# Kernel tuning notes

Hardware: AMD Instinct MI355X
Metric: run time of the kernel (lower is better)

The kernel has to match this reference:

```python
import jax, jax.numpy as jnp
import numpy as np

B, L, HID = 2, 2048, 512
NUM_HEADS = 8
HEAD_DIM = HID // NUM_HEADS
GAP_ROWS = 33   # num_time_gap_buckets + 1
DUR_ROWS = 17   # num_duration_buckets + 1
NEG = -1e9      # finite stand-in for -inf (grad-safe, masked probs ~0)


def setup_inputs() -> dict:
    key = jax.random.key(0)
    ks = jax.random.split(key, 16)
    s = 1.0 / np.sqrt(HID)
    x = jax.random.normal(ks[0], (B, L, HID), dtype=jnp.float32)
    attention_mask = jax.random.randint(ks[1], (B, L), 0, 2, dtype=jnp.int32)
    time_gap_bucket_ids = jax.random.randint(ks[2], (B, L), 0, GAP_ROWS, dtype=jnp.int32)
    duration_bucket_ids = jax.random.randint(ks[3], (B, L), 0, DUR_ROWS, dtype=jnp.int32)
    Wq = jax.random.normal(ks[4], (HID, HID), dtype=jnp.float32) * s
    bq = jnp.zeros((HID,), jnp.float32)
    Wk = jax.random.normal(ks[5], (HID, HID), dtype=jnp.float32) * s
    bk = jnp.zeros((HID,), jnp.float32)
    Wv = jax.random.normal(ks[6], (HID, HID), dtype=jnp.float32) * s
    bv = jnp.zeros((HID,), jnp.float32)
    Wo = jax.random.normal(ks[7], (HID, HID), dtype=jnp.float32) * s
    bo = jnp.zeros((HID,), jnp.float32)
    # bias tables: padding_idx=0 row kept at zero, rest random for a meaningful test
    gap_emb = jax.random.normal(ks[8], (GAP_ROWS, NUM_HEADS), dtype=jnp.float32) * 0.1
    gap_emb = gap_emb.at[0].set(0.0)
    dur_emb = jax.random.normal(ks[9], (DUR_ROWS, NUM_HEADS), dtype=jnp.float32) * 0.1
    dur_emb = dur_emb.at[0].set(0.0)
    return dict(x=x, attention_mask=attention_mask,
                time_gap_bucket_ids=time_gap_bucket_ids,
                duration_bucket_ids=duration_bucket_ids,
                Wq=Wq, bq=bq, Wk=Wk, bk=bk, Wv=Wv, bv=bv, Wo=Wo, bo=bo,
                gap_emb=gap_emb, dur_emb=dur_emb)


def reference(x, attention_mask, time_gap_bucket_ids, duration_bucket_ids,
              Wq, bq, Wk, bk, Wv, bv, Wo, bo, gap_emb, dur_emb):
    b, l, hid = x.shape
    h, d = NUM_HEADS, HEAD_DIM
    def split_heads(t):  # (B,L,HID) -> (B,h,L,d)
        return t.reshape(b, l, h, d).transpose(0, 2, 1, 3)
    Q = split_heads(x @ Wq + bq)
    K = split_heads(x @ Wk + bk)
    V = split_heads(x @ Wv + bv)
    scores = jnp.einsum('bhqd,bhkd->bhqk', Q, K) / jnp.sqrt(jnp.float32(d))
    # relative time-gap bias: (B,L,L) bucket lookup -> (B,h,L,L)
    rel = jnp.abs(time_gap_bucket_ids[:, :, None] - time_gap_bucket_ids[:, None, :])
    rel = jnp.clip(rel, 0, GAP_ROWS - 1)
    gap_bias = gap_emb[rel]                       # (B,L,L,h)
    scores = scores + gap_bias.transpose(0, 3, 1, 2)
    # per-key duration bias: (B,L,h) -> (B,h,1,L)
    dur_bias = dur_emb[duration_bucket_ids]       # (B,L,h)
    scores = scores + dur_bias.transpose(0, 2, 1)[:, :, None, :]
    pad = (attention_mask == 0)[:, None, None, :]  # (B,1,1,L) over keys
    scores = jnp.where(pad, NEG, scores)
    attn = jax.nn.softmax(scores, axis=-1)
    out = jnp.einsum('bhqk,bhkd->bhqd', attn, V)
    out = out.transpose(0, 2, 1, 3).reshape(b, l, hid)
    return out @ Wo + bo
```

## Files before the change

### kernel.cpp

```cpp
#include <hip/hip_runtime.h>
#include <cmath>

typedef unsigned short u16;
typedef unsigned int   u32;
typedef __attribute__((ext_vector_type(2))) unsigned uintx2;
typedef __attribute__((ext_vector_type(4))) float    floatx4;
typedef __attribute__((ext_vector_type(4))) unsigned uintx4;
typedef __attribute__((ext_vector_type(8))) __bf16   bf16x8;

#define MFMA16(a, b, c) __builtin_amdgcn_mfma_f32_16x16x32_bf16((a), (b), (c), 0, 0, 0)

__device__ __forceinline__ u16 f2bf(float f) {
    union { float f; u32 u; } v; v.f = f;
    u32 u = v.u;
    return (u16)((u + 0x7FFFu + ((u >> 16) & 1u)) >> 16);
}

__device__ __forceinline__ bf16x8 ld_frag(const u16* p) {
    uintx4 t = *(const uintx4*)p;
    return __builtin_bit_cast(bf16x8, t);
}

#if __has_builtin(__builtin_amdgcn_exp2f)
#define EXP2F(x) __builtin_amdgcn_exp2f(x)
#else
#define EXP2F(x) exp2f(x)
#endif

typedef __attribute__((address_space(3))) unsigned       lds_u32;
typedef __attribute__((address_space(1))) const unsigned glb_u32;
__device__ __forceinline__ void gl_lds16(const void* g, void* l) {
    __builtin_amdgcn_global_load_lds((glb_u32*)(uintptr_t)g, (lds_u32*)(uintptr_t)l, 16, 0, 0);
}

#define LOG2E   1.4426950408889634f
#define QSCALE  0.18033688011112043f

__global__ __launch_bounds__(256) void prep_kernel(
        const float* __restrict__ x, const int* __restrict__ gap_ids,
        const int* __restrict__ dur_ids, const int* __restrict__ amask,
        const float* __restrict__ gap_emb, const float* __restrict__ dur_emb,
        const float* __restrict__ Wq, const float* __restrict__ Wk,
        const float* __restrict__ Wv, const float* __restrict__ Wo,
        u16* __restrict__ Xb, u16* __restrict__ Qe, u16* __restrict__ Ke,
        u16* __restrict__ WqT, u16* __restrict__ WkT,
        u16* __restrict__ WvT, u16* __restrict__ WoT) {
    __shared__ u16 T[64][72];
    int bid = blockIdx.x, tid = threadIdx.x;
    if (bid < 1024) {
        int idx = bid * 256 + tid;
        const float* src = x + (size_t)idx * 8;
        uintx4 o;
        o.x = f2bf(src[0]) | ((u32)f2bf(src[1]) << 16);
        o.y = f2bf(src[2]) | ((u32)f2bf(src[3]) << 16);
        o.z = f2bf(src[4]) | ((u32)f2bf(src[5]) << 16);
        o.w = f2bf(src[6]) | ((u32)f2bf(src[7]) << 16);
        *(uintx4*)(Xb + (size_t)idx * 8) = o;
    } else if (bid < 2048) {
        int ri = (bid - 1024) * 32 + (tid >> 3);
        int l = ri & 2047;
        int b = ri >> 14;
        int ch = tid & 7;
        int gq = gap_ids[b * 2048 + l];
        u16 lg = f2bf(LOG2E);
        u16 vals[8];
        for (int e = 0; e < 8; e++) {
            int j = ch * 8 + e;
            vals[e] = (j == gq || j == 33) ? lg : (u16)0;
        }
        *(uintx4*)(Qe + (size_t)ri * 128 + (8 + ch) * 8) = *(uintx4*)vals;
    } else if (bid < 3072) {
        int ri = (bid - 2048) * 32 + (tid >> 3);
        int bh = ri >> 11, l = ri & 2047;
        int b = bh >> 3, h = bh & 7;
        int ch = tid & 7;
        int gk = gap_ids[b * 2048 + l];
        int did = dur_ids[b * 2048 + l];
        int msk = amask[b * 2048 + l];
        float kval = msk ? dur_emb[did * 8 + h] : -1e9f;
        u16 vals[8];
        for (int e = 0; e < 8; e++) {
            int j = ch * 8 + e;
            float v;
            if (j <= 32) { int d = j - gk; d = d < 0 ? -d : d; v = gap_emb[d * 8 + h]; }
            else if (j == 33) v = kval;
            else v = 0.f;
            vals[e] = f2bf(v);
        }
        int phys = 8 | (ch ^ (l & 7));
        *(uintx4*)(Ke + (size_t)ri * 128 + phys * 8) = *(uintx4*)vals;
    } else {
        int bid2 = bid - 3072;
        int mat = bid2 >> 6, t8 = bid2 & 63;
        int n0 = (t8 & 7) * 64, k0 = (t8 >> 3) * 64;
        const float* W = (mat == 0) ? Wq : (mat == 1) ? Wk : (mat == 2) ? Wv : Wo;
        u16* WT = (mat == 0) ? WqT : (mat == 1) ? WkT : (mat == 2) ? WvT : WoT;
        int r = tid >> 4, cq = tid & 15;
        for (int rr = 0; rr < 4; rr++) {
            int row = r + rr * 16;
            floatx4 s = *(const floatx4*)&W[(size_t)(k0 + row) * 512 + n0 + cq * 4];
            T[cq * 4 + 0][row] = f2bf(s.x);
            T[cq * 4 + 1][row] = f2bf(s.y);
            T[cq * 4 + 2][row] = f2bf(s.z);
            T[cq * 4 + 3][row] = f2bf(s.w);
        }
        __syncthreads();
        for (int p = 0; p < 2; p++) {
            int idx = p * 256 + tid;
            int c = idx >> 3, ch = idx & 7;
            *(uintx4*)&WT[(size_t)(n0 + c) * 512 + k0 + ch * 8] = *(const uintx4*)&T[c][ch * 8];
        }
    }
}

__global__ __launch_bounds__(256) void gemm_qkv(
        const u16* __restrict__ Xb,
        const u16* __restrict__ WqT, const u16* __restrict__ WkT, const u16* __restrict__ WvT,
        const float* __restrict__ bq, const float* __restrict__ bk, const float* __restrict__ bv,
        u16* __restrict__ Qe, u16* __restrict__ Ke, u16* __restrict__ Vt) {
    __shared__ u16 smem[12288];
    u16* As = smem;
    u16* Bs = smem + 8192;

    int tid = threadIdx.x;
    int m0 = blockIdx.x * 128;
    int gy = blockIdx.y;
    int mat = gy >> 3, hh = gy & 7;
    int ncol0 = hh * 64;
    const u16* Bt = (mat == 0) ? WqT : (mat == 1) ? WkT : WvT;
    const float* bias = (mat == 0) ? bq : (mat == 1) ? bk : bv;

    int lane = tid & 63, w = tid >> 6, lo = lane & 15, hi = lane >> 4;
    int wm = w >> 1, wn = w & 1;
    floatx4 acc[4][2] = {};

    for (int kb = 0; kb < 8; kb++) {
        int k0 = kb * 64;
        __syncthreads();
        for (int it = 0; it < 4; it++) {
            int c = it * 256 + tid;
            int row = c >> 3, ch = c & 7;
            gl_lds16((const char*)Xb + ((size_t)(m0 + row) * 512 + k0) * 2 + ch * 16,
                     (char*)As + c * 16);
        }
        for (int it = 0; it < 2; it++) {
            int c = it * 256 + tid;
            int row = c >> 3, ch = c & 7;
            gl_lds16((const char*)Bt + ((size_t)(ncol0 + row) * 512 + k0) * 2 + ch * 16,
                     (char*)Bs + c * 16);
        }
        __syncthreads();
        for (int s = 0; s < 2; s++) {
            bf16x8 a[4], b[2];
            for (int i = 0; i < 4; i++)
                a[i] = ld_frag(&As[(64 * wm + 16 * i + lo) * 64 + s * 32 + hi * 8]);
            for (int j = 0; j < 2; j++)
                b[j] = ld_frag(&Bs[(32 * wn + 16 * j + lo) * 64 + s * 32 + hi * 8]);
            for (int i = 0; i < 4; i++)
                for (int j = 0; j < 2; j++)
                    acc[i][j] = MFMA16(a[i], b[j], acc[i][j]);
        }
    }

    int bb = m0 >> 11, l0 = m0 & 2047;
    __syncthreads();

    if (mat < 2) {
        u16* Ot = smem;
        for (int j = 0; j < 2; j++) {
            int col = 32 * wn + 16 * j + lo;
            float bval = bias[ncol0 + col];
            for (int i = 0; i < 4; i++) {
                int row = 64 * wm + 16 * i + 4 * hi;
                for (int r = 0; r < 4; r++) {
                    float v = acc[i][j][r] + bval;
                    if (mat == 0) v *= QSCALE;
                    Ot[(row + r) * 72 + col] = f2bf(v);
                }
            }
        }
        __syncthreads();
        for (int p = 0; p < 4; p++) {
            int cc = p * 256 + tid;
            int row = cc >> 3, ch = cc & 7;
            int lrow = l0 + row;
            size_t rowi = (size_t)(bb * 8 + hh) * 2048 + lrow;
            int ch2 = (mat == 1) ? (ch ^ (lrow & 7)) : ch;
            u16* dstp = (mat == 0) ? Qe : Ke;
            *(uintx4*)(dstp + rowi * 128 + ch2 * 8) = *(const uintx4*)(Ot + row * 72 + ch * 8);
        }
    } else {
        u16* Ot = smem;
        for (int j = 0; j < 2; j++) {
            int dc = 32 * wn + 16 * j + lo;
            float bval = bias[ncol0 + dc];
            for (int i = 0; i < 4; i++) {
                int row = 64 * wm + 16 * i + 4 * hi;
                for (int r = 0; r < 4; r++)
                    Ot[dc * 136 + row + r] = f2bf(acc[i][j][r] + bval);
            }
        }
        __syncthreads();
        for (int p = 0; p < 4; p++) {
            int cc4 = p * 256 + tid;
            int dc = cc4 >> 4, c16 = cc4 & 15;
            int g64 = c16 >> 3, phys = c16 & 7;
            int mlog = phys ^ (dc & 7);
            int g = mlog >> 2, q = mlog & 3;
            int base = g64 * 64 + 32 * g + 4 * q;
            uintx2 lo4 = *(const uintx2*)(Ot + dc * 136 + base);
            uintx2 hi4 = *(const uintx2*)(Ot + dc * 136 + base + 16);
            uintx4 t; t.x = lo4.x; t.y = lo4.y; t.z = hi4.x; t.w = hi4.y;
            size_t dst = ((size_t)(bb * 8 + hh) * 64 + dc) * 2048 + l0 + g64 * 64 + phys * 8;
            *(uintx4*)(Vt + dst) = t;
        }
    }
}

__global__ __launch_bounds__(256, 3) void flash_attn(
        const u16* __restrict__ Qe, const u16* __restrict__ Ke, const u16* __restrict__ Vt,
        float* __restrict__ Opart, float* __restrict__ Lpart) {
    __shared__ u16 Ks[2][64 * 128];
    __shared__ u16 Vs[2][64 * 64];

    int tid = threadIdx.x, lane = tid & 63, w = tid >> 6, lo = lane & 15, hi = lane >> 4;
    int qt2 = blockIdx.x, bh = blockIdx.y, sp = blockIdx.z;
    int sw = lo & 7;

    bf16x8 bq_[2][4];
    for (int g = 0; g < 2; g++) {
        size_t qrow = ((size_t)bh * 2048 + qt2 * 128 + g * 64 + 16 * w + lo) * 128;
        for (int kc = 0; kc < 4; kc++) bq_[g][kc] = ld_frag(&Qe[qrow + kc * 32 + hi * 8]);
    }

    floatx4 O[2][4] = {};
    floatx4 Lacc[2] = {};
    uintx4 onesu; onesu.x = 0x3F803F80u; onesu.y = 0x3F803F80u; onesu.z = 0x3F803F80u; onesu.w = 0x3F803F80u;
    bf16x8 ones = __builtin_bit_cast(bf16x8, onesu);

    const u16* KeB = Ke + (size_t)bh * 2048 * 128;
    const u16* VtB = Vt + (size_t)bh * 64 * 2048;

    int kbeg = sp * 16, kend = kbeg + 16;

#define STAGE(KT, BUF) do {                                                        \
        int k0_ = (KT) * 64;                                                       \
        const char* gk_ = (const char*)(KeB + (size_t)k0_ * 128);                  \
        char* lk_ = (char*)Ks[BUF];                                                \
        for (int r2 = 0; r2 < 4; r2++)                                             \
            gl_lds16(gk_ + r2 * 4096 + tid * 16, lk_ + r2 * 4096 + tid * 16);      \
        for (int p2 = 0; p2 < 2; p2++) {                                           \
            int c_ = p2 * 256 + tid;                                               \
            int row_ = c_ >> 3, ch_ = c_ & 7;                                      \
            gl_lds16((const char*)(VtB + (size_t)row_ * 2048 + k0_) + ch_ * 16,    \
                     (char*)Vs[BUF] + c_ * 16);                                    \
        }                                                                          \
    } while (0)

    int cur = 0;
    STAGE(kbeg, 0);
    for (int kt = kbeg; kt < kend; kt++) {
        __syncthreads();
        if (kt + 1 < kend) STAGE(kt + 1, cur ^ 1);

        const u16* Ksc = Ks[cur];
        const u16* Vsc = Vs[cur];

        floatx4 sf[2][4] = {};
        for (int t = 0; t < 4; t++) {
            const u16* krow = &Ksc[(16 * t + lo) * 128];
            for (int kc = 0; kc < 4; kc++) {
                int cc = kc * 4 + hi;
                int pc = (cc & 8) | ((cc & 7) ^ sw);
                bf16x8 a = ld_frag(&krow[pc * 8]);
                sf[0][t] = MFMA16(a, bq_[0][kc], sf[0][t]);
                sf[1][t] = MFMA16(a, bq_[1][kc], sf[1][t]);
            }
        }

        bf16x8 af[2][2];
        for (int g = 0; g < 2; g++) {
            u32 pk[4][2];
            for (int t = 0; t < 4; t++) {
                float p0 = EXP2F(sf[g][t][0]);
                float p1 = EXP2F(sf[g][t][1]);
                float p2 = EXP2F(sf[g][t][2]);
                float p3 = EXP2F(sf[g][t][3]);
                u32 u0 = __builtin_bit_cast(u32, p0) + 0x8000u;
                u32 u1 = __builtin_bit_cast(u32, p1) + 0x8000u;
                u32 u2 = __builtin_bit_cast(u32, p2) + 0x8000u;
                u32 u3 = __builtin_bit_cast(u32, p3) + 0x8000u;
                pk[t][0] = __builtin_amdgcn_perm(u1, u0, 0x07060302);
                pk[t][1] = __builtin_amdgcn_perm(u3, u2, 0x07060302);
            }
            for (int tp = 0; tp < 2; tp++) {
                uintx4 av;
                av.x = pk[2 * tp][0]; av.y = pk[2 * tp][1];
                av.z = pk[2 * tp + 1][0]; av.w = pk[2 * tp + 1][1];
                af[g][tp] = __builtin_bit_cast(bf16x8, av);
            }
        }

        for (int tp = 0; tp < 2; tp++) {
            Lacc[0] = MFMA16(af[0][tp], ones, Lacc[0]);
            Lacc[1] = MFMA16(af[1][tp], ones, Lacc[1]);
            for (int u = 0; u < 4; u++) {
                const u16* vrow = &Vsc[(16 * u + lo) * 64];
                int m = (4 * tp + hi) ^ sw;
                bf16x8 bv = ld_frag(&vrow[m * 8]);
                O[0][u] = MFMA16(af[0][tp], bv, O[0][u]);
                O[1][u] = MFMA16(af[1][tp], bv, O[1][u]);
            }
        }
        cur ^= 1;
    }
#undef STAGE

    for (int g = 0; g < 2; g++) {
        int qt = 2 * qt2 + g;
        size_t obase = (((size_t)sp * 16 + bh) * 32 + qt) * 4096;
        for (int u = 0; u < 4; u++)
            for (int r = 0; r < 4; r++)
                Opart[obase + (size_t)(16 * w + 4 * hi + r) * 64 + 16 * u + lo] = O[g][u][r];
        if (lo == 0) {
            size_t lbase = (((size_t)sp * 16 + bh) * 32 + qt) * 64;
            for (int r = 0; r < 4; r++) Lpart[lbase + 16 * w + 4 * hi + r] = Lacc[g][r];
        }
    }
}

__global__ __launch_bounds__(256) void combine_kernel(const float* __restrict__ Opart,
                                                      const float* __restrict__ Lpart,
                                                      u16* __restrict__ Ob) {
    int idx = blockIdx.x * 256 + threadIdx.x;
    int d4 = idx & 15;
    int q = (idx >> 4) & 2047;
    int bh = idx >> 15;
    int qt = q >> 6, qr = q & 63;
    size_t b0 = ((size_t)bh * 32 + qt) * 4096 + qr * 64 + d4 * 4;
    floatx4 o0 = *(const floatx4*)&Opart[b0];
    floatx4 o1 = *(const floatx4*)&Opart[b0 + 2097152];
    size_t lb = ((size_t)bh * 32 + qt) * 64 + qr;
    float rl = 1.0f / (Lpart[lb] + Lpart[lb + 32768]);
    uintx2 pk2;
    pk2.x = f2bf((o0.x + o1.x) * rl) | ((u32)f2bf((o0.y + o1.y) * rl) << 16);
    pk2.y = f2bf((o0.z + o1.z) * rl) | ((u32)f2bf((o0.w + o1.w) * rl) << 16);
    int bb = bh >> 3, h = bh & 7;
    *(uintx2*)&Ob[((size_t)(bb * 2048 + q)) * 512 + h * 64 + d4 * 4] = pk2;
}

__global__ __launch_bounds__(256) void gemm_out(
        const u16* __restrict__ Ob, const u16* __restrict__ WoT,
        const float* __restrict__ bo, float* __restrict__ out) {
    __shared__ u16 As[64][72];
    __shared__ u16 Bs[64][72];
    int tid = threadIdx.x;
    int m0 = blockIdx.x * 64;
    int n0 = blockIdx.y * 64;
    int lane = tid & 63, w = tid >> 6, lo = lane & 15, hi = lane >> 4;
    floatx4 acc[4] = {};

    for (int kb = 0; kb < 8; kb++) {
        __syncthreads();
        for (int c = tid; c < 512; c += 256) {
            int row = c >> 3, cc = c & 7;
            *(uintx4*)&As[row][cc * 8] =
                *(const uintx4*)&Ob[(size_t)(m0 + row) * 512 + kb * 64 + cc * 8];
            *(uintx4*)&Bs[row][cc * 8] =
                *(const uintx4*)&WoT[(size_t)(n0 + row) * 512 + kb * 64 + cc * 8];
        }
        __syncthreads();
        for (int s = 0; s < 2; s++) {
            bf16x8 a = ld_frag(&As[16 * w + lo][8 * hi + 32 * s]);
            for (int t = 0; t < 4; t++) {
                bf16x8 b = ld_frag(&Bs[16 * t + lo][8 * hi + 32 * s]);
                acc[t] = MFMA16(a, b, acc[t]);
            }
        }
    }
    for (int t = 0; t < 4; t++) {
        int n = n0 + 16 * t + lo;
        float bval = bo[n];
        for (int r = 0; r < 4; r++) {
            int mrow = m0 + 16 * w + 4 * hi + r;
            out[(size_t)mrow * 512 + n] = acc[t][r] + bval;
        }
    }
}

extern "C" void kernel_launch(void* const* d_in, const int* in_sizes, int n_in,
                              void* d_out, int out_size, void* d_ws, size_t ws_size,
                              hipStream_t stream) {
    const float* x     = (const float*)d_in[0];
    const int*   amask = (const int*)d_in[1];
    const int*   gids  = (const int*)d_in[2];
    const int*   dids  = (const int*)d_in[3];
    const float* Wq    = (const float*)d_in[4];
    const float* bq    = (const float*)d_in[5];
    const float* Wk    = (const float*)d_in[6];
    const float* bk    = (const float*)d_in[7];
    const float* Wv    = (const float*)d_in[8];
    const float* bv    = (const float*)d_in[9];
    const float* Wo    = (const float*)d_in[10];
    const float* bo    = (const float*)d_in[11];
    const float* gap_emb = (const float*)d_in[12];
    const float* dur_emb = (const float*)d_in[13];
    float* out = (float*)d_out;

    char* ws = (char*)d_ws;
    u16*   Qe    = (u16*)(ws + 0);
    u16*   Ke    = (u16*)(ws + 8388608);
    u16*   Vt    = (u16*)(ws + 16777216);
    float* Opart = (float*)(ws + 20971520);
    float* Lpart = (float*)(ws + 37748736);
    u16*   Ob    = (u16*)(ws + 38010880);
    u16*   WoT   = (u16*)(ws + 42205184);
    u16*   Xb    = (u16*)(ws + 20971520);
    u16*   WqT   = (u16*)(ws + 25165824);
    u16*   WkT   = (u16*)(ws + 25690112);
    u16*   WvT   = (u16*)(ws + 26214400);

    hipLaunchKernelGGL(prep_kernel, dim3(3328), dim3(256), 0, stream,
                       x, gids, dids, amask, gap_emb, dur_emb,
                       Wq, Wk, Wv, Wo, Xb, Qe, Ke, WqT, WkT, WvT, WoT);
    hipLaunchKernelGGL(gemm_qkv, dim3(32, 24), dim3(256), 0, stream,
                       Xb, WqT, WkT, WvT, bq, bk, bv, Qe, Ke, Vt);
    hipLaunchKernelGGL(flash_attn, dim3(16, 16, 2), dim3(256), 0, stream,
                       Qe, Ke, Vt, Opart, Lpart);
    hipLaunchKernelGGL(combine_kernel, dim3(2048), dim3(256), 0, stream,
                       Opart, Lpart, Ob);
    hipLaunchKernelGGL(gemm_out, dim3(64, 8), dim3(256), 0, stream,
                       Ob, WoT, bo, out);
}
```

Measured before the change: 145.0 us.

## Widen flash attention query tile to 256 rows and split keys four ways

Each flash attention block now processes four 64-row query groups (256 queries) instead of two, so every K/V tile staged in shared memory is reused by twice as many MFMAs. The key range is split into four chunks instead of two, which keeps the grid at 512 blocks, and the combine kernel now sums four partials. Double buffering of K/V is dropped in favour of a single buffer with two barriers per step, and the occupancy hint falls from 3 to 2 blocks. The price is more register pressure, no overlap between loads and compute, and twice the partial-output traffic through the combine step.

```diff
diff --git a/kernel.cpp b/kernel.cpp
--- a/kernel.cpp
+++ b/kernel.cpp
@@ -217,107 +217,106 @@
     }
 }
 
-__global__ __launch_bounds__(256, 3) void flash_attn(
+__global__ __launch_bounds__(256, 2) void flash_attn(
         const u16* __restrict__ Qe, const u16* __restrict__ Ke, const u16* __restrict__ Vt,
         float* __restrict__ Opart, float* __restrict__ Lpart) {
-    __shared__ u16 Ks[2][64 * 128];
-    __shared__ u16 Vs[2][64 * 64];
+    __shared__ u16 Ks[64 * 128];
+    __shared__ u16 Vs[64 * 64];
 
     int tid = threadIdx.x, lane = tid & 63, w = tid >> 6, lo = lane & 15, hi = lane >> 4;
-    int qt2 = blockIdx.x, bh = blockIdx.y, sp = blockIdx.z;
+    int qt4 = blockIdx.x, bh = blockIdx.y, sp = blockIdx.z;
     int sw = lo & 7;
 
-    bf16x8 bq_[2][4];
-    for (int g = 0; g < 2; g++) {
-        size_t qrow = ((size_t)bh * 2048 + qt2 * 128 + g * 64 + 16 * w + lo) * 128;
+    bf16x8 bq_[4][4];
+    for (int g = 0; g < 4; g++) {
+        size_t qrow = ((size_t)bh * 2048 + qt4 * 256 + g * 64 + 16 * w + lo) * 128;
         for (int kc = 0; kc < 4; kc++) bq_[g][kc] = ld_frag(&Qe[qrow + kc * 32 + hi * 8]);
     }
 
-    floatx4 O[2][4] = {};
-    floatx4 Lacc[2] = {};
+    floatx4 O[4][4] = {};
+    floatx4 Lacc[4] = {};
     uintx4 onesu; onesu.x = 0x3F803F80u; onesu.y = 0x3F803F80u; onesu.z = 0x3F803F80u; onesu.w = 0x3F803F80u;
     bf16x8 ones = __builtin_bit_cast(bf16x8, onesu);
 
     const u16* KeB = Ke + (size_t)bh * 2048 * 128;
     const u16* VtB = Vt + (size_t)bh * 64 * 2048;
 
-    int kbeg = sp * 16, kend = kbeg + 16;
-
-#define STAGE(KT, BUF) do {                                                        \
-        int k0_ = (KT) * 64;                                                       \
-        const char* gk_ = (const char*)(KeB + (size_t)k0_ * 128);                  \
-        char* lk_ = (char*)Ks[BUF];                                                \
-        for (int r2 = 0; r2 < 4; r2++)                                             \
-            gl_lds16(gk_ + r2 * 4096 + tid * 16, lk_ + r2 * 4096 + tid * 16);      \
-        for (int p2 = 0; p2 < 2; p2++) {                                           \
-            int c_ = p2 * 256 + tid;                                               \
-            int row_ = c_ >> 3, ch_ = c_ & 7;                                      \
-            gl_lds16((const char*)(VtB + (size_t)row_ * 2048 + k0_) + ch_ * 16,    \
-                     (char*)Vs[BUF] + c_ * 16);                                    \
-        }                                                                          \
-    } while (0)
-
-    int cur = 0;
-    STAGE(kbeg, 0);
+    int kbeg = sp * 8, kend = kbeg + 8;
+
     for (int kt = kbeg; kt < kend; kt++) {
-        __syncthreads();
-        if (kt + 1 < kend) STAGE(kt + 1, cur ^ 1);
-
-        const u16* Ksc = Ks[cur];
-        const u16* Vsc = Vs[cur];
-
-        floatx4 sf[2][4] = {};
+        int k0 = kt * 64;
+        __syncthreads();
+        {
+            const char* gk = (const char*)(KeB + (size_t)k0 * 128);
+            for (int r2 = 0; r2 < 4; r2++)
+                gl_lds16(gk + r2 * 4096 + tid * 16, (char*)Ks + r2 * 4096 + tid * 16);
+        }
+        {
+            for (int p2 = 0; p2 < 2; p2++) {
+                int c = p2 * 256 + tid;
+                int row = c >> 3, ch = c & 7;
+                gl_lds16((const char*)(VtB + (size_t)row * 2048 + k0) + ch * 16,
+                         (char*)Vs + c * 16);
+            }
+        }
+        __syncthreads();
+
+        u32 pk[4][4][2];
         for (int t = 0; t < 4; t++) {
-            const u16* krow = &Ksc[(16 * t + lo) * 128];
+            const u16* krow = &Ks[(16 * t + lo) * 128];
+            bf16x8 a[4];
             for (int kc = 0; kc < 4; kc++) {
                 int cc = kc * 4 + hi;
                 int pc = (cc & 8) | ((cc & 7) ^ sw);
-                bf16x8 a = ld_frag(&krow[pc * 8]);
-                sf[0][t] = MFMA16(a, bq_[0][kc], sf[0][t]);
-                sf[1][t] = MFMA16(a, bq_[1][kc], sf[1][t]);
-            }
-        }
-
-        bf16x8 af[2][2];
-        for (int g = 0; g < 2; g++) {
-            u32 pk[4][2];
-            for (int t = 0; t < 4; t++) {
-                float p0 = EXP2F(sf[g][t][0]);
-                float p1 = EXP2F(sf[g][t][1]);
-                float p2 = EXP2F(sf[g][t][2]);
-                float p3 = EXP2F(sf[g][t][3]);
+                a[kc] = ld_frag(&krow[pc * 8]);
+            }
+            floatx4 sf[4] = {};
+            for (int kc = 0; kc < 4; kc++) {
+                sf[0] = MFMA16(a[kc], bq_[0][kc], sf[0]);
+                sf[1] = MFMA16(a[kc], bq_[1][kc], sf[1]);
+                sf[2] = MFMA16(a[kc], bq_[2][kc], sf[2]);
+                sf[3] = MFMA16(a[kc], bq_[3][kc], sf[3]);
+            }
+            for (int g = 0; g < 4; g++) {
+                float p0 = EXP2F(sf[g][0]);
+                float p1 = EXP2F(sf[g][1]);
+                float p2 = EXP2F(sf[g][2]);
+                float p3 = EXP2F(sf[g][3]);
                 u32 u0 = __builtin_bit_cast(u32, p0) + 0x8000u;
                 u32 u1 = __builtin_bit_cast(u32, p1) + 0x8000u;
                 u32 u2 = __builtin_bit_cast(u32, p2) + 0x8000u;
                 u32 u3 = __builtin_bit_cast(u32, p3) + 0x8000u;
-                pk[t][0] = __builtin_amdgcn_perm(u1, u0, 0x07060302);
-                pk[t][1] = __builtin_amdgcn_perm(u3, u2, 0x07060302);
-            }
-            for (int tp = 0; tp < 2; tp++) {
+                pk[g][t][0] = __builtin_amdgcn_perm(u1, u0, 0x07060302);
+                pk[g][t][1] = __builtin_amdgcn_perm(u3, u2, 0x07060302);
+            }
+        }
+
+        for (int tp = 0; tp < 2; tp++) {
+            bf16x8 af[4];
+            for (int g = 0; g < 4; g++) {
                 uintx4 av;
-                av.x = pk[2 * tp][0]; av.y = pk[2 * tp][1];
-                av.z = pk[2 * tp + 1][0]; av.w = pk[2 * tp + 1][1];
-                af[g][tp] = __builtin_bit_cast(bf16x8, av);
-            }
-        }
-
-        for (int tp = 0; tp < 2; tp++) {
-            Lacc[0] = MFMA16(af[0][tp], ones, Lacc[0]);
-            Lacc[1] = MFMA16(af[1][tp], ones, Lacc[1]);
+                av.x = pk[g][2 * tp][0]; av.y = pk[g][2 * tp][1];
+                av.z = pk[g][2 * tp + 1][0]; av.w = pk[g][2 * tp + 1][1];
+                af[g] = __builtin_bit_cast(bf16x8, av);
+            }
+            Lacc[0] = MFMA16(af[0], ones, Lacc[0]);
+            Lacc[1] = MFMA16(af[1], ones, Lacc[1]);
+            Lacc[2] = MFMA16(af[2], ones, Lacc[2]);
+            Lacc[3] = MFMA16(af[3], ones, Lacc[3]);
             for (int u = 0; u < 4; u++) {
-                const u16* vrow = &Vsc[(16 * u + lo) * 64];
+                const u16* vrow = &Vs[(16 * u + lo) * 64];
                 int m = (4 * tp + hi) ^ sw;
                 bf16x8 bv = ld_frag(&vrow[m * 8]);
-                O[0][u] = MFMA16(af[0][tp], bv, O[0][u]);
-                O[1][u] = MFMA16(af[1][tp], bv, O[1][u]);
-            }
-        }
-        cur ^= 1;
-    }
-#undef STAGE
-
-    for (int g = 0; g < 2; g++) {
-        int qt = 2 * qt2 + g;
+                O[0][u] = MFMA16(af[0], bv, O[0][u]);
+                O[1][u] = MFMA16(af[1], bv, O[1][u]);
+                O[2][u] = MFMA16(af[2], bv, O[2][u]);
+                O[3][u] = MFMA16(af[3], bv, O[3][u]);
+            }
+        }
+    }
+
+    for (int g = 0; g < 4; g++) {
+        int qt = 4 * qt4 + g;
         size_t obase = (((size_t)sp * 16 + bh) * 32 + qt) * 4096;
         for (int u = 0; u < 4; u++)
             for (int r = 0; r < 4; r++)
@@ -340,11 +339,13 @@
     size_t b0 = ((size_t)bh * 32 + qt) * 4096 + qr * 64 + d4 * 4;
     floatx4 o0 = *(const floatx4*)&Opart[b0];
     floatx4 o1 = *(const floatx4*)&Opart[b0 + 2097152];
+    floatx4 o2 = *(const floatx4*)&Opart[b0 + 4194304];
+    floatx4 o3 = *(const floatx4*)&Opart[b0 + 6291456];
     size_t lb = ((size_t)bh * 32 + qt) * 64 + qr;
-    float rl = 1.0f / (Lpart[lb] + Lpart[lb + 32768]);
+    float rl = 1.0f / (Lpart[lb] + Lpart[lb + 32768] + Lpart[lb + 65536] + Lpart[lb + 98304]);
     uintx2 pk2;
-    pk2.x = f2bf((o0.x + o1.x) * rl) | ((u32)f2bf((o0.y + o1.y) * rl) << 16);
-    pk2.y = f2bf((o0.z + o1.z) * rl) | ((u32)f2bf((o0.w + o1.w) * rl) << 16);
+    pk2.x = f2bf((o0.x + o1.x + o2.x + o3.x) * rl) | ((u32)f2bf((o0.y + o1.y + o2.y + o3.y) * rl) << 16);
+    pk2.y = f2bf((o0.z + o1.z + o2.z + o3.z) * rl) | ((u32)f2bf((o0.w + o1.w + o2.w + o3.w) * rl) << 16);
     int bb = bh >> 3, h = bh & 7;
     *(uintx2*)&Ob[((size_t)(bb * 2048 + q)) * 512 + h * 64 + d4 * 4] = pk2;
 }
@@ -412,9 +413,9 @@
     u16*   Ke    = (u16*)(ws + 8388608);
     u16*   Vt    = (u16*)(ws + 16777216);
     float* Opart = (float*)(ws + 20971520);
-    float* Lpart = (float*)(ws + 37748736);
-    u16*   Ob    = (u16*)(ws + 38010880);
-    u16*   WoT   = (u16*)(ws + 42205184);
+    float* Lpart = (float*)(ws + 54525952);
+    u16*   Ob    = (u16*)(ws + 55050240);
+    u16*   WoT   = (u16*)(ws + 59244544);
     u16*   Xb    = (u16*)(ws + 20971520);
     u16*   WqT   = (u16*)(ws + 25165824);
     u16*   WkT   = (u16*)(ws + 25690112);
@@ -425,7 +426,7 @@
                        Wq, Wk, Wv, Wo, Xb, Qe, Ke, WqT, WkT, WvT, WoT);
     hipLaunchKernelGGL(gemm_qkv, dim3(32, 24), dim3(256), 0, stream,
                        Xb, WqT, WkT, WvT, bq, bk, bv, Qe, Ke, Vt);
-    hipLaunchKernelGGL(flash_attn, dim3(16, 16, 2), dim3(256), 0, stream,
+    hipLaunchKernelGGL(flash_attn, dim3(8, 16, 4), dim3(256), 0, stream,
                        Qe, Ke, Vt, Opart, Lpart);
     hipLaunchKernelGGL(combine_kernel, dim3(2048), dim3(256), 0, stream,
                        Opart, Lpart, Ob);
```

Result: slower. 152.1 us (+4.8%).

## Double-buffer LDS staging in QKV and output GEMMs with async global-to-LDS loads

Applied to the files above, without the earlier changes.

Gives the QKV projection GEMM and the output GEMM two LDS buffers. The loads for the next k-block are issued right after the barrier, so they overlap the MFMA work on the current block. The output GEMM moves from register-staged loads to direct global-to-LDS loads with an unpadded 64-wide layout. An explicit vmcnt(0) wait is added before each barrier, including in the attention loop, so the async LDS writes are complete before use. This doubles LDS per block and drops the padding, which may cost occupancy and add bank conflicts in the output GEMM.

```diff
diff --git a/kernel.cpp b/kernel.cpp
--- a/kernel.cpp
+++ b/kernel.cpp
@@ -32,6 +32,8 @@
 __device__ __forceinline__ void gl_lds16(const void* g, void* l) {
     __builtin_amdgcn_global_load_lds((glb_u32*)(uintptr_t)g, (lds_u32*)(uintptr_t)l, 16, 0, 0);
 }
+
+#define DRAIN() asm volatile("s_waitcnt vmcnt(0)" ::: "memory")
 
 #define LOG2E   1.4426950408889634f
 #define QSCALE  0.18033688011112043f
@@ -118,9 +120,7 @@
         const u16* __restrict__ WqT, const u16* __restrict__ WkT, const u16* __restrict__ WvT,
         const float* __restrict__ bq, const float* __restrict__ bk, const float* __restrict__ bv,
         u16* __restrict__ Qe, u16* __restrict__ Ke, u16* __restrict__ Vt) {
-    __shared__ u16 smem[12288];
-    u16* As = smem;
-    u16* Bs = smem + 8192;
+    __shared__ u16 smem[2][12288];
 
     int tid = threadIdx.x;
     int m0 = blockIdx.x * 128;
@@ -134,22 +134,29 @@
     int wm = w >> 1, wn = w & 1;
     floatx4 acc[4][2] = {};
 
+#define QSTAGE(KB, BUF) do {                                                            \
+        int k0_ = (KB) * 64;                                                            \
+        for (int it = 0; it < 4; it++) {                                                \
+            int c = it * 256 + tid;                                                     \
+            int row = c >> 3, ch = c & 7;                                               \
+            gl_lds16((const char*)Xb + ((size_t)(m0 + row) * 512 + k0_) * 2 + ch * 16,  \
+                     (char*)(smem[BUF]) + c * 16);                                      \
+        }                                                                               \
+        for (int it = 0; it < 2; it++) {                                                \
+            int c = it * 256 + tid;                                                     \
+            int row = c >> 3, ch = c & 7;                                               \
+            gl_lds16((const char*)Bt + ((size_t)(ncol0 + row) * 512 + k0_) * 2 + ch * 16,\
+                     (char*)(smem[BUF] + 8192) + c * 16);                               \
+        }                                                                               \
+    } while (0)
+
+    QSTAGE(0, 0);
     for (int kb = 0; kb < 8; kb++) {
-        int k0 = kb * 64;
-        __syncthreads();
-        for (int it = 0; it < 4; it++) {
-            int c = it * 256 + tid;
-            int row = c >> 3, ch = c & 7;
-            gl_lds16((const char*)Xb + ((size_t)(m0 + row) * 512 + k0) * 2 + ch * 16,
-                     (char*)As + c * 16);
-        }
-        for (int it = 0; it < 2; it++) {
-            int c = it * 256 + tid;
-            int row = c >> 3, ch = c & 7;
-            gl_lds16((const char*)Bt + ((size_t)(ncol0 + row) * 512 + k0) * 2 + ch * 16,
-                     (char*)Bs + c * 16);
-        }
-        __syncthreads();
+        DRAIN();
+        __syncthreads();
+        if (kb + 1 < 8) QSTAGE(kb + 1, (kb + 1) & 1);
+        const u16* As = smem[kb & 1];
+        const u16* Bs = smem[kb & 1] + 8192;
         for (int s = 0; s < 2; s++) {
             bf16x8 a[4], b[2];
             for (int i = 0; i < 4; i++)
@@ -161,12 +168,13 @@
                     acc[i][j] = MFMA16(a[i], b[j], acc[i][j]);
         }
     }
+#undef QSTAGE
 
     int bb = m0 >> 11, l0 = m0 & 2047;
     __syncthreads();
 
     if (mat < 2) {
-        u16* Ot = smem;
+        u16* Ot = smem[0];
         for (int j = 0; j < 2; j++) {
             int col = 32 * wn + 16 * j + lo;
             float bval = bias[ncol0 + col];
@@ -190,7 +198,7 @@
             *(uintx4*)(dstp + rowi * 128 + ch2 * 8) = *(const uintx4*)(Ot + row * 72 + ch * 8);
         }
     } else {
-        u16* Ot = smem;
+        u16* Ot = smem[0];
         for (int j = 0; j < 2; j++) {
             int dc = 32 * wn + 16 * j + lo;
             float bval = bias[ncol0 + dc];
@@ -260,6 +268,7 @@
     int cur = 0;
     STAGE(kbeg, 0);
     for (int kt = kbeg; kt < kend; kt++) {
+        DRAIN();
         __syncthreads();
         if (kt + 1 < kend) STAGE(kt + 1, cur ^ 1);
 
@@ -352,32 +361,46 @@
 __global__ __launch_bounds__(256) void gemm_out(
         const u16* __restrict__ Ob, const u16* __restrict__ WoT,
         const float* __restrict__ bo, float* __restrict__ out) {
-    __shared__ u16 As[64][72];
-    __shared__ u16 Bs[64][72];
+    __shared__ u16 smem[2][8192];
     int tid = threadIdx.x;
     int m0 = blockIdx.x * 64;
     int n0 = blockIdx.y * 64;
     int lane = tid & 63, w = tid >> 6, lo = lane & 15, hi = lane >> 4;
     floatx4 acc[4] = {};
 
+#define OSTAGE(KB, BUF) do {                                                            \
+        int k0_ = (KB) * 64;                                                            \
+        for (int it = 0; it < 2; it++) {                                                \
+            int c = it * 256 + tid;                                                     \
+            int row = c >> 3, ch = c & 7;                                               \
+            gl_lds16((const char*)Ob + ((size_t)(m0 + row) * 512 + k0_) * 2 + ch * 16,  \
+                     (char*)(smem[BUF]) + c * 16);                                      \
+        }                                                                               \
+        for (int it = 0; it < 2; it++) {                                                \
+            int c = it * 256 + tid;                                                     \
+            int row = c >> 3, ch = c & 7;                                               \
+            gl_lds16((const char*)WoT + ((size_t)(n0 + row) * 512 + k0_) * 2 + ch * 16, \
+                     (char*)(smem[BUF] + 4096) + c * 16);                               \
+        }                                                                               \
+    } while (0)
+
+    OSTAGE(0, 0);
     for (int kb = 0; kb < 8; kb++) {
-        __syncthreads();
-        for (int c = tid; c < 512; c += 256) {
-            int row = c >> 3, cc = c & 7;
-            *(uintx4*)&As[row][cc * 8] =
-                *(const uintx4*)&Ob[(size_t)(m0 + row) * 512 + kb * 64 + cc * 8];
-            *(uintx4*)&Bs[row][cc * 8] =
-                *(const uintx4*)&WoT[(size_t)(n0 + row) * 512 + kb * 64 + cc * 8];
-        }
-        __syncthreads();
+        DRAIN();
+        __syncthreads();
+        if (kb + 1 < 8) OSTAGE(kb + 1, (kb + 1) & 1);
+        const u16* As = smem[kb & 1];
+        const u16* Bs = smem[kb & 1] + 4096;
         for (int s = 0; s < 2; s++) {
-            bf16x8 a = ld_frag(&As[16 * w + lo][8 * hi + 32 * s]);
+            bf16x8 a = ld_frag(&As[(16 * w + lo) * 64 + s * 32 + hi * 8]);
             for (int t = 0; t < 4; t++) {
-                bf16x8 b = ld_frag(&Bs[16 * t + lo][8 * hi + 32 * s]);
+                bf16x8 b = ld_frag(&Bs[(16 * t + lo) * 64 + s * 32 + hi * 8]);
                 acc[t] = MFMA16(a, b, acc[t]);
             }
         }
     }
+#undef OSTAGE
+
     for (int t = 0; t < 4; t++) {
         int n = n0 + 16 * t + lo;
         float bval = bo[n];
```

Result: faster. 141.9 us (-2.2%).
